# Kernel optimization log

Measured on AMD Instinct MI355X. Metric: run time of the kernel, lower is better.

## Reference

```python
import jax, jax.numpy as jnp
import numpy as np
import math

# Model dims (DeepSeek-V2 style, N reduced to 32 heads)
S = 2048       # tokens (single causal prefill sequence)
H = 5120       # hidden size
N = 32         # heads
P = 128        # qk nope head dim
R = 64         # qk rope head dim
V = 128        # v head dim
LQ = 1536      # q lora rank
LKV = 512      # kv lora rank
QK = P + R
EPS = 1e-6
BASE = 10000.0
FACTOR = 40.0
ORIG_MAX = 4096
BETA_FAST, BETA_SLOW = 32, 1

def _yarn_get_mscale(scale, mscale=1.0):
    if scale <= 1:
        return 1.0
    return 0.1 * mscale * math.log(scale) + 1.0

# softmax scale includes mscale^2 (mscale_all_dim=1.0)
SCALE = (QK ** -0.5) * _yarn_get_mscale(FACTOR, 1.0) ** 2
# cos/sin multiplier: yarn_get_mscale(f, mscale)/yarn_get_mscale(f, mscale_all_dim) = 1.0 here
MSCALE_COS = _yarn_get_mscale(FACTOR, 1.0) / _yarn_get_mscale(FACTOR, 1.0)

def _yarn_inv_freq():
    half = R // 2
    pos_freqs = BASE ** (np.arange(0, R, 2, dtype=np.float64) / R)
    extrapolation = 1.0 / pos_freqs
    interpolation = 1.0 / (FACTOR * pos_freqs)
    def corr_dim(n_rot):
        return R * math.log(ORIG_MAX / (n_rot * 2 * math.pi)) / (2 * math.log(BASE))
    low = max(math.floor(corr_dim(BETA_FAST)), 0)
    high = min(math.ceil(corr_dim(BETA_SLOW)), R - 1)
    ramp = np.clip((np.arange(half, dtype=np.float64) - low) / max(high - low, 0.001), 0, 1)
    mask = 1.0 - ramp  # extrapolation mask
    inv_freq = interpolation * (1 - mask) + extrapolation * mask
    return jnp.asarray(inv_freq, dtype=jnp.float32)

INV_FREQ = _yarn_inv_freq()  # (R//2,)

def _rms_norm(x, w):
    var = jnp.mean(x * x, axis=-1, keepdims=True)
    return x * jax.lax.rsqrt(var + EPS) * w

def _apply_rope_gptj(x, cos, sin):
    # non-neox (interleaved-pair) rotation; x: (..., R), cos/sin broadcastable (..., R//2)
    x1 = x[..., 0::2]
    x2 = x[..., 1::2]
    o1 = x1 * cos - x2 * sin
    o2 = x2 * cos + x1 * sin
    return jnp.stack([o1, o2], axis=-1).reshape(x.shape)

def setup_inputs() -> dict:
    key = jax.random.key(0)
    ks = jax.random.split(key, 6)
    s = 0.02
    return {
        "positions": jnp.arange(S, dtype=jnp.int64 if jax.config.jax_enable_x64 else jnp.int32),
        "hidden_states": jax.random.normal(ks[0], (S, H), dtype=jnp.float32),
        "w_qa": jax.random.normal(ks[1], (H, LQ), dtype=jnp.float32) * s,
        "q_a_ln_w": jnp.ones((LQ,), dtype=jnp.float32),
        "w_qb": jax.random.normal(ks[2], (LQ, N * QK), dtype=jnp.float32) * s,
        "w_kva": jax.random.normal(ks[3], (H, LKV + R), dtype=jnp.float32) * s,
        "kv_a_ln_w": jnp.ones((LKV,), dtype=jnp.float32),
        "w_kvb": jax.random.normal(ks[4], (LKV, N * (P + V)), dtype=jnp.float32) * s,
        "w_o": jax.random.normal(ks[5], (N * V, H), dtype=jnp.float32) * s,
    }

def reference(positions, hidden_states, w_qa, q_a_ln_w, w_qb, w_kva, kv_a_ln_w, w_kvb, w_o):
    # --- Q path: down-proj -> RMSNorm -> up-proj ---
    q_lat = _rms_norm(hidden_states @ w_qa, q_a_ln_w)             # (S, LQ)
    q = (q_lat @ w_qb).reshape(S, N, QK)                          # (S, N, P+R)
    q_nope, q_pe = q[..., :P], q[..., P:]
    # --- KV path: joint down-proj, split, norm kv_a, up-proj ---
    latent = hidden_states @ w_kva                                # (S, LKV+R)
    kv_a, k_pe = latent[:, :LKV], latent[:, LKV:]
    kv_a = _rms_norm(kv_a, kv_a_ln_w)
    kv = (kv_a @ w_kvb).reshape(S, N, P + V)
    k_nope, v = kv[..., :P], kv[..., P:]
    # --- partial RoPE (yarn, non-neox) on q_pe, k_pe ---
    freqs = positions.astype(jnp.float32)[:, None] * INV_FREQ     # (S, R//2)
    cos = jnp.cos(freqs) * MSCALE_COS
    sin = jnp.sin(freqs) * MSCALE_COS
    q_pe = _apply_rope_gptj(q_pe, cos[:, None, :], sin[:, None, :])  # (S, N, R)
    k_pe = _apply_rope_gptj(k_pe, cos, sin)                          # (S, R)
    # --- assemble q, k and run causal MHA ---
    q_full = jnp.concatenate([q_nope, q_pe], axis=-1)             # (S, N, QK)
    k_full = jnp.concatenate(
        [k_nope, jnp.broadcast_to(k_pe[:, None, :], (S, N, R))], axis=-1)
    scores = jnp.einsum('snd,tnd->nst', q_full, k_full) * SCALE   # (N, S, S)
    causal = jnp.tril(jnp.ones((S, S), dtype=bool))
    scores = jnp.where(causal[None], scores, jnp.finfo(scores.dtype).min)
    probs = jax.nn.softmax(scores, axis=-1)
    attn = jnp.einsum('nst,tnv->snv', probs, v)                   # (S, N, V)
    out = attn.reshape(S, N * V) @ w_o                            # (S, H)
    return out
```

## Files before the change

### kernel.cpp

```cpp
#include <hip/hip_runtime.h>
#include <hip/hip_bf16.h>
#include <math.h>

#define DEVI __device__ __forceinline__

typedef __bf16 bf16x8 __attribute__((ext_vector_type(8)));
typedef float f32x4 __attribute__((ext_vector_type(4)));

#define MFMA16(a, b, c) __builtin_amdgcn_mfma_f32_16x16x32_bf16((a), (b), (c), 0, 0, 0)

struct RopeConsts { float inv_freq[32]; };

DEVI float bfbits2f(unsigned int u) { union { unsigned int i; float f; } x; x.i = u << 16; return x.f; }
DEVI unsigned short f2bfbits(float f) {
    __hip_bfloat16 h = __float2bfloat16(f);
    unsigned short u; __builtin_memcpy(&u, &h, 2); return u;
}

DEVI void gl_lds16(const __hip_bfloat16* g, __hip_bfloat16* l) {
    __builtin_amdgcn_global_load_lds((const __attribute__((address_space(1))) void*)g,
                                     (__attribute__((address_space(3))) void*)l, 16, 0, 0);
}

__global__ void k_cvt_f32_bf16(const float* __restrict__ s, __hip_bfloat16* __restrict__ d, long n) {
    long i = ((long)blockIdx.x * 256 + threadIdx.x) * 4;
    if (i >= n) return;
    float4 f = *(const float4*)(s + i);
    ushort4 o = make_ushort4(f2bfbits(f.x), f2bfbits(f.y), f2bfbits(f.z), f2bfbits(f.w));
    *(ushort4*)((unsigned short*)d + i) = o;
}

struct TransBatch {
    const float* src[5];
    __hip_bfloat16* dst[5];
    int K[5], N[5], nbx[5];
    int boff[6];
};

__global__ __launch_bounds__(256)
void k_transpose_batch(TransBatch tbp) {
    __shared__ float tile[128][33];
    const int b = blockIdx.x;
    int seg = 0;
    if (b >= tbp.boff[1]) seg = 1;
    if (b >= tbp.boff[2]) seg = 2;
    if (b >= tbp.boff[3]) seg = 3;
    if (b >= tbp.boff[4]) seg = 4;
    const int local = b - tbp.boff[seg];
    const int nbx = tbp.nbx[seg];
    const int K = tbp.K[seg], N = tbp.N[seg];
    const float* __restrict__ src = tbp.src[seg];
    __hip_bfloat16* __restrict__ dst = tbp.dst[seg];
    const int nb = (local % nbx) * 32, kb = (local / nbx) * 128;

    const int tx = threadIdx.x & 31, ty = threadIdx.x >> 5;
    #pragma unroll
    for (int r = 0; r < 128; r += 8) {
        int k = kb + r + ty, n = nb + tx;
        tile[r + ty][tx] = (n < N) ? src[(size_t)k * N + n] : 0.0f;
    }
    __syncthreads();
    const int nl = threadIdx.x >> 3;
    const int kq = (threadIdx.x & 7) << 4;
    unsigned short* drow = (unsigned short*)(dst + (size_t)(nb + nl) * K + kb + kq);
    #pragma unroll
    for (int j4 = 0; j4 < 4; ++j4) {
        ushort4 o;
        o.x = f2bfbits(tile[kq + j4 * 4 + 0][nl]);
        o.y = f2bfbits(tile[kq + j4 * 4 + 1][nl]);
        o.z = f2bfbits(tile[kq + j4 * 4 + 2][nl]);
        o.w = f2bfbits(tile[kq + j4 * 4 + 3][nl]);
        *(ushort4*)(drow + j4 * 4) = o;
    }
}

DEVI void storeC(float* C, size_t i, float v) { C[i] = v; }
DEVI void storeC(__hip_bfloat16* C, size_t i, float v) { C[i] = __float2bfloat16(v); }

template <int NI, typename CT>
__global__ __launch_bounds__(512, 2)
void k_gemm128w(const __hip_bfloat16* __restrict__ A, int lda,
                const __hip_bfloat16* __restrict__ Bt,
                CT* __restrict__ C, int N, int K, float alpha) {
    extern __shared__ __hip_bfloat16 sm[];
    __hip_bfloat16* As = sm;
    __hip_bfloat16* Bs = sm + 16384;
    const int tid = threadIdx.x;
    const int lane = tid & 63, wave = tid >> 6;
    const int wm = wave >> 2, wn = wave & 3;
    const size_t bm = (size_t)blockIdx.y * 128, bn = (size_t)blockIdx.x * (64 * NI);

    const int srow8 = lane >> 3;
    const int sch = (lane & 7) ^ srow8;
    const __hip_bfloat16* Agb = A + (bm + wave * 8 + srow8) * (size_t)lda + (sch << 3);
    const __hip_bfloat16* Bgb = Bt + (bn + wave * 8 + srow8) * (size_t)K + (sch << 3);
    __hip_bfloat16* AsW = As + wave * 512;
    __hip_bfloat16* BsW = Bs + wave * 512;

    auto stage = [&](int buf, int kt) {
        #pragma unroll
        for (int i = 0; i < 2; ++i)
            gl_lds16(Agb + (size_t)i * 64 * lda + kt, AsW + buf * 8192 + i * 4096);
        #pragma unroll
        for (int i = 0; i < NI; ++i)
            gl_lds16(Bgb + (size_t)i * 64 * K + kt, BsW + buf * (NI * 4096) + i * 4096);
    };

    int aoff[4], boff[NI];
    #pragma unroll
    for (int mi = 0; mi < 4; ++mi) {
        int r = wm * 64 + mi * 16 + (lane & 15);
        aoff[mi] = r * 64 + (((lane >> 4) ^ (r & 7)) << 3);
    }
    #pragma unroll
    for (int ni = 0; ni < NI; ++ni) {
        int r = wn * (16 * NI) + ni * 16 + (lane & 15);
        boff[ni] = r * 64 + (((lane >> 4) ^ (r & 7)) << 3);
    }

    f32x4 acc[4][NI] = {};
    const int NT = K >> 6;

    stage(0, 0);
    stage(1, 64);
    asm volatile("s_waitcnt vmcnt(%0)" :: "n"(2 + NI) : "memory");
    __builtin_amdgcn_s_barrier();
    __builtin_amdgcn_sched_barrier(0);

    for (int t = 0; t < NT; ++t) {
        const int b = t & 1;
        const __hip_bfloat16* Ab = As + b * 8192;
        const __hip_bfloat16* Bb = Bs + b * (NI * 4096);
        bf16x8 af[4], bfr[NI];

        #pragma unroll
        for (int mi = 0; mi < 4; ++mi) af[mi] = *(const bf16x8*)(Ab + aoff[mi]);
        #pragma unroll
        for (int ni = 0; ni < NI; ++ni) bfr[ni] = *(const bf16x8*)(Bb + boff[ni]);
        __builtin_amdgcn_s_setprio(1);
        #pragma unroll
        for (int mi = 0; mi < 4; ++mi)
            #pragma unroll
            for (int ni = 0; ni < NI; ++ni)
                acc[mi][ni] = MFMA16(af[mi], bfr[ni], acc[mi][ni]);
        __builtin_amdgcn_s_setprio(0);

        #pragma unroll
        for (int mi = 0; mi < 4; ++mi) af[mi] = *(const bf16x8*)(Ab + (aoff[mi] ^ 32));
        #pragma unroll
        for (int ni = 0; ni < NI; ++ni) bfr[ni] = *(const bf16x8*)(Bb + (boff[ni] ^ 32));
        __builtin_amdgcn_s_setprio(1);
        #pragma unroll
        for (int mi = 0; mi < 4; ++mi)
            #pragma unroll
            for (int ni = 0; ni < NI; ++ni)
                acc[mi][ni] = MFMA16(af[mi], bfr[ni], acc[mi][ni]);
        __builtin_amdgcn_s_setprio(0);

        __builtin_amdgcn_sched_barrier(0);
        __builtin_amdgcn_s_barrier();
        if (t + 2 < NT) {
            stage(b, (t + 2) << 6);
            asm volatile("s_waitcnt vmcnt(%0)" :: "n"(2 + NI) : "memory");
        } else {
            asm volatile("s_waitcnt vmcnt(0)" ::: "memory");
        }
        __builtin_amdgcn_s_barrier();
        __builtin_amdgcn_sched_barrier(0);
    }

    const int row0 = (int)bm + wm * 64 + ((lane >> 4) << 2);
    const int col0 = (int)bn + wn * (16 * NI) + (lane & 15);
    #pragma unroll
    for (int mi = 0; mi < 4; ++mi)
        #pragma unroll
        for (int ni = 0; ni < NI; ++ni)
            #pragma unroll
            for (int r = 0; r < 4; ++r)
                storeC(C, (size_t)(row0 + mi * 16 + r) * N + (col0 + ni * 16), acc[mi][ni][r] * alpha);
}

template <typename CT>
__global__ __launch_bounds__(256, 2)
void k_gemm128p(const __hip_bfloat16* __restrict__ A, int lda,
                const __hip_bfloat16* __restrict__ Bt,
                CT* __restrict__ C, int N, int K, float alpha) {
    __shared__ __hip_bfloat16 As[2 * 8192];
    __shared__ __hip_bfloat16 Bs[2 * 8192];
    const int tid = threadIdx.x;
    const int lane = tid & 63, wave = tid >> 6;
    const int wm = wave >> 1, wn = wave & 1;
    const size_t bm = (size_t)blockIdx.y * 128, bn = (size_t)blockIdx.x * 128;

    const int srow8 = lane >> 3;
    const int sch = (lane & 7) ^ srow8;
    const __hip_bfloat16* Agb = A + (bm + wave * 8 + srow8) * (size_t)lda + (sch << 3);
    const __hip_bfloat16* Bgb = Bt + (bn + wave * 8 + srow8) * (size_t)K + (sch << 3);
    __hip_bfloat16* AsW = As + wave * 512;
    __hip_bfloat16* BsW = Bs + wave * 512;

    auto stage = [&](int buf, int kt) {
        #pragma unroll
        for (int i = 0; i < 4; ++i)
            gl_lds16(Agb + (size_t)i * 32 * lda + kt, AsW + buf * 8192 + i * 2048);
        #pragma unroll
        for (int i = 0; i < 4; ++i)
            gl_lds16(Bgb + (size_t)i * 32 * K + kt, BsW + buf * 8192 + i * 2048);
    };

    int aoff[4], boff[4];
    #pragma unroll
    for (int mi = 0; mi < 4; ++mi) {
        int r = wm * 64 + mi * 16 + (lane & 15);
        aoff[mi] = r * 64 + (((lane >> 4) ^ (r & 7)) << 3);
    }
    #pragma unroll
    for (int ni = 0; ni < 4; ++ni) {
        int r = wn * 64 + ni * 16 + (lane & 15);
        boff[ni] = r * 64 + (((lane >> 4) ^ (r & 7)) << 3);
    }

    f32x4 acc[4][4] = {};
    const int NT = K >> 6;

    stage(0, 0);
    stage(1, 64);
    asm volatile("s_waitcnt vmcnt(8)" ::: "memory");
    __builtin_amdgcn_s_barrier();
    __builtin_amdgcn_sched_barrier(0);

    for (int t = 0; t < NT; ++t) {
        const int b = t & 1;
        const __hip_bfloat16* Ab = As + b * 8192;
        const __hip_bfloat16* Bb = Bs + b * 8192;
        bf16x8 af[4], bfr[4];

        #pragma unroll
        for (int mi = 0; mi < 4; ++mi) af[mi] = *(const bf16x8*)(Ab + aoff[mi]);
        #pragma unroll
        for (int ni = 0; ni < 4; ++ni) bfr[ni] = *(const bf16x8*)(Bb + boff[ni]);
        __builtin_amdgcn_s_setprio(1);
        #pragma unroll
        for (int mi = 0; mi < 4; ++mi)
            #pragma unroll
            for (int ni = 0; ni < 4; ++ni)
                acc[mi][ni] = MFMA16(af[mi], bfr[ni], acc[mi][ni]);
        __builtin_amdgcn_s_setprio(0);

        #pragma unroll
        for (int mi = 0; mi < 4; ++mi) af[mi] = *(const bf16x8*)(Ab + (aoff[mi] ^ 32));
        #pragma unroll
        for (int ni = 0; ni < 4; ++ni) bfr[ni] = *(const bf16x8*)(Bb + (boff[ni] ^ 32));
        __builtin_amdgcn_s_setprio(1);
        #pragma unroll
        for (int mi = 0; mi < 4; ++mi)
            #pragma unroll
            for (int ni = 0; ni < 4; ++ni)
                acc[mi][ni] = MFMA16(af[mi], bfr[ni], acc[mi][ni]);
        __builtin_amdgcn_s_setprio(0);

        __builtin_amdgcn_sched_barrier(0);
        __builtin_amdgcn_s_barrier();
        if (t + 2 < NT) {
            stage(b, (t + 2) << 6);
            asm volatile("s_waitcnt vmcnt(8)" ::: "memory");
        } else {
            asm volatile("s_waitcnt vmcnt(0)" ::: "memory");
        }
        __builtin_amdgcn_s_barrier();
        __builtin_amdgcn_sched_barrier(0);
    }

    const int row0 = (int)bm + wm * 64 + ((lane >> 4) << 2);
    const int col0 = (int)bn + wn * 64 + (lane & 15);
    #pragma unroll
    for (int mi = 0; mi < 4; ++mi)
        #pragma unroll
        for (int ni = 0; ni < 4; ++ni)
            #pragma unroll
            for (int r = 0; r < 4; ++r)
                storeC(C, (size_t)(row0 + mi * 16 + r) * N + (col0 + ni * 16), acc[mi][ni][r] * alpha);
}

template <typename CT>
__global__ __launch_bounds__(512, 2)
void k_gemm256(const __hip_bfloat16* __restrict__ A, int lda,
               const __hip_bfloat16* __restrict__ Bt,
               CT* __restrict__ C, int N, int K) {
    extern __shared__ __hip_bfloat16 sm[];
    __hip_bfloat16* As = sm;
    __hip_bfloat16* Bs = sm + 32768;
    const int tid = threadIdx.x;
    const int lane = tid & 63, wave = tid >> 6;
    const int wm = wave >> 2, wn = wave & 3;
    const size_t bm = (size_t)blockIdx.y * 256, bn = (size_t)blockIdx.x * 256;

    const int srow8 = lane >> 3;
    const int sch = (lane & 7) ^ srow8;
    const __hip_bfloat16* Agb = A + (bm + wave * 8 + srow8) * (size_t)lda + (sch << 3);
    const __hip_bfloat16* Bgb = Bt + (bn + wave * 8 + srow8) * (size_t)K + (sch << 3);
    __hip_bfloat16* AsW = As + wave * 512;
    __hip_bfloat16* BsW = Bs + wave * 512;

    auto stage = [&](int buf, int kt) {
        #pragma unroll
        for (int i = 0; i < 4; ++i)
            gl_lds16(Agb + (size_t)i * 64 * lda + kt, AsW + buf * 16384 + i * 4096);
        #pragma unroll
        for (int i = 0; i < 4; ++i)
            gl_lds16(Bgb + (size_t)i * 64 * K + kt, BsW + buf * 16384 + i * 4096);
    };

    int aoff[8], boff[4];
    #pragma unroll
    for (int mi = 0; mi < 8; ++mi) {
        int r = wm * 128 + mi * 16 + (lane & 15);
        aoff[mi] = r * 64 + (((lane >> 4) ^ (r & 7)) << 3);
    }
    #pragma unroll
    for (int ni = 0; ni < 4; ++ni) {
        int r = wn * 64 + ni * 16 + (lane & 15);
        boff[ni] = r * 64 + (((lane >> 4) ^ (r & 7)) << 3);
    }

    f32x4 acc[8][4] = {};
    const int NT = K >> 6;

    stage(0, 0);
    stage(1, 64);
    asm volatile("s_waitcnt vmcnt(8)" ::: "memory");
    __builtin_amdgcn_s_barrier();
    __builtin_amdgcn_sched_barrier(0);

    for (int t = 0; t < NT; ++t) {
        const int b = t & 1;
        const __hip_bfloat16* Ab = As + b * 16384;
        const __hip_bfloat16* Bb = Bs + b * 16384;
        bf16x8 af[8], bfr[4];

        #pragma unroll
        for (int mi = 0; mi < 8; ++mi) af[mi] = *(const bf16x8*)(Ab + aoff[mi]);
        #pragma unroll
        for (int ni = 0; ni < 4; ++ni) bfr[ni] = *(const bf16x8*)(Bb + boff[ni]);
        __builtin_amdgcn_s_setprio(1);
        #pragma unroll
        for (int mi = 0; mi < 8; ++mi)
            #pragma unroll
            for (int ni = 0; ni < 4; ++ni)
                acc[mi][ni] = MFMA16(af[mi], bfr[ni], acc[mi][ni]);
        __builtin_amdgcn_s_setprio(0);

        #pragma unroll
        for (int mi = 0; mi < 8; ++mi) af[mi] = *(const bf16x8*)(Ab + (aoff[mi] ^ 32));
        #pragma unroll
        for (int ni = 0; ni < 4; ++ni) bfr[ni] = *(const bf16x8*)(Bb + (boff[ni] ^ 32));
        __builtin_amdgcn_s_setprio(1);
        #pragma unroll
        for (int mi = 0; mi < 8; ++mi)
            #pragma unroll
            for (int ni = 0; ni < 4; ++ni)
                acc[mi][ni] = MFMA16(af[mi], bfr[ni], acc[mi][ni]);
        __builtin_amdgcn_s_setprio(0);

        __builtin_amdgcn_sched_barrier(0);
        __builtin_amdgcn_s_barrier();
        if (t + 2 < NT) {
            stage(b, (t + 2) << 6);
            asm volatile("s_waitcnt vmcnt(8)" ::: "memory");
        } else {
            asm volatile("s_waitcnt vmcnt(0)" ::: "memory");
        }
        __builtin_amdgcn_s_barrier();
        __builtin_amdgcn_sched_barrier(0);
    }

    const int row0 = (int)bm + wm * 128 + ((lane >> 4) << 2);
    const int col0 = (int)bn + wn * 64 + (lane & 15);
    #pragma unroll
    for (int mi = 0; mi < 8; ++mi)
        #pragma unroll
        for (int ni = 0; ni < 4; ++ni)
            #pragma unroll
            for (int r = 0; r < 4; ++r)
                storeC(C, (size_t)(row0 + mi * 16 + r) * N + (col0 + ni * 16), acc[mi][ni][r]);
}

__global__ __launch_bounds__(256)
void k_rmsnorm2(__hip_bfloat16* base, int stride,
                const float* __restrict__ w0, int D0,
                int off1, const float* __restrict__ w1, int D1) {
    const int row = blockIdx.x;
    const int which = blockIdx.y;
    const float* w = which ? w1 : w0;
    const int D = which ? D1 : D0;
    unsigned int* xr = (unsigned int*)(base + (size_t)row * stride + (which ? off1 : 0));
    const int tid = threadIdx.x;
    const int n2 = D >> 1;
    float a[3], b[3];
    float ss = 0.0f;
    int c = 0;
    for (int i = tid; i < n2; i += 256) {
        unsigned int v = xr[i];
        float lo = bfbits2f(v & 0xffffu), hi = bfbits2f(v >> 16);
        a[c] = lo; b[c] = hi; ++c;
        ss += lo * lo + hi * hi;
    }
    #pragma unroll
    for (int d = 1; d < 64; d <<= 1) ss += __shfl_xor(ss, d, 64);
    __shared__ float red[4];
    if ((tid & 63) == 0) red[tid >> 6] = ss;
    __syncthreads();
    ss = red[0] + red[1] + red[2] + red[3];
    const float rs = rsqrtf(ss / (float)D + 1e-6f);
    c = 0;
    for (int i = tid; i < n2; i += 256) {
        float lo = a[c] * rs * w[2 * i], hi = b[c] * rs * w[2 * i + 1];
        xr[i] = (unsigned int)f2bfbits(lo) | ((unsigned int)f2bfbits(hi) << 16);
        ++c;
    }
}

__global__ __launch_bounds__(256)
void k_rope(__hip_bfloat16* __restrict__ q, __hip_bfloat16* __restrict__ latent, int lstride,
            const int* __restrict__ positions, RopeConsts rc) {
    __shared__ float2 scs[32];
    const int s = blockIdx.x, tid = threadIdx.x;
    if (tid < 32) {
        float fr = (float)positions[s] * rc.inv_freq[tid];
        float sn, cn;
        sincosf(fr, &sn, &cn);
        scs[tid] = make_float2(cn, sn);
    }
    __syncthreads();
    #pragma unroll
    for (int p = tid; p < 1024; p += 256) {
        int head = p >> 5, i = p & 31;
        float2 c = scs[i];
        unsigned int* b = (unsigned int*)(q + (size_t)s * 6144 + head * 192 + 128 + 2 * i);
        unsigned int v = *b;
        float x1 = bfbits2f(v & 0xffffu), x2 = bfbits2f(v >> 16);
        float o1 = x1 * c.x - x2 * c.y, o2 = x2 * c.x + x1 * c.y;
        *b = (unsigned int)f2bfbits(o1) | ((unsigned int)f2bfbits(o2) << 16);
    }
    if (tid < 32) {
        float2 c = scs[tid];
        unsigned int* b = (unsigned int*)(latent + (size_t)s * lstride + 512 + 2 * tid);
        unsigned int v = *b;
        float x1 = bfbits2f(v & 0xffffu), x2 = bfbits2f(v >> 16);
        float o1 = x1 * c.x - x2 * c.y, o2 = x2 * c.x + x1 * c.y;
        *b = (unsigned int)f2bfbits(o1) | ((unsigned int)f2bfbits(o2) << 16);
    }
}

__global__ __launch_bounds__(256)
void k_vtrans(const __hip_bfloat16* __restrict__ kv, __hip_bfloat16* __restrict__ vt) {
    __shared__ unsigned int tile[128][33];
    const int h = blockIdx.z, t0 = blockIdx.x * 128, v0 = blockIdx.y * 32;
    const int tx = threadIdx.x & 31, ty = threadIdx.x >> 5;
    const unsigned short* kvu = (const unsigned short*)kv;
    #pragma unroll
    for (int r = 0; r < 128; r += 8) {
        int t = t0 + r + ty;
        tile[r + ty][tx] = kvu[(size_t)t * 8192 + h * 256 + 128 + v0 + tx];
    }
    __syncthreads();
    const int vl = threadIdx.x >> 3;
    const int tq = (threadIdx.x & 7) << 4;
    unsigned short* drow = (unsigned short*)(vt + ((size_t)h * 128 + v0 + vl) * 2048 + t0 + tq);
    #pragma unroll
    for (int j4 = 0; j4 < 4; ++j4) {
        ushort4 o;
        o.x = (unsigned short)tile[tq + j4 * 4 + 0][vl];
        o.y = (unsigned short)tile[tq + j4 * 4 + 1][vl];
        o.z = (unsigned short)tile[tq + j4 * 4 + 2][vl];
        o.w = (unsigned short)tile[tq + j4 * 4 + 3][vl];
        *(ushort4*)(drow + j4 * 4) = o;
    }
}

template <int NBUF>
__global__ __launch_bounds__(512, 1)
void k_attn(const __hip_bfloat16* __restrict__ q,
            const __hip_bfloat16* __restrict__ kv,
            const __hip_bfloat16* __restrict__ latent,
            int lstride,
            const __hip_bfloat16* __restrict__ vt,
            __hip_bfloat16* __restrict__ attnout) {
    extern __shared__ __hip_bfloat16 smem[];
    __hip_bfloat16* KN = smem;
    __hip_bfloat16* KP = KN + NBUF * 8192;
    __hip_bfloat16* VT = KP + NBUF * 4096;
    __hip_bfloat16* P  = VT + NBUF * 8192;

    const int h = blockIdx.x & 31;
    const int pr = (int)(blockIdx.x >> 5);
    const int tid = threadIdx.x;
    const int lane = tid & 63, wave = tid >> 6;
    const int l15 = lane & 15, rquad = lane >> 4;
    const int qrw0 = pr * 128 + wave * 16;
    const int qrw1 = (15 - pr) * 128 + wave * 16;
    const int nt0 = 2 * pr + 2;
    const int nt  = 2 * (15 - pr) + 2;

    auto stage = [&](int buf, int t0) {
        #pragma unroll
        for (int p = 0; p < 2; ++p) {
            int s = p * 512 + tid;
            int row = s >> 4, ch = s & 15;
            gl_lds16(kv + (size_t)(t0 + row) * 8192 + h * 256 + ((ch ^ (row & 7)) << 3),
                     KN + buf * 8192 + p * 4096 + wave * 512);
        }
        {
            int row = tid >> 3, ch = tid & 7;
            gl_lds16(latent + (size_t)(t0 + row) * lstride + 512 + ((ch ^ (row & 7)) << 3),
                     KP + buf * 4096 + wave * 512);
        }
        #pragma unroll
        for (int p = 0; p < 2; ++p) {
            int s = p * 512 + tid;
            int row = s >> 3, ch = s & 7;
            gl_lds16(vt + ((size_t)h * 128 + row) * 2048 + t0 + ((ch ^ (row & 7)) << 3),
                     VT + buf * 8192 + p * 4096 + wave * 512);
        }
    };

    bf16x8 qf[2][6];
    {
        const __hip_bfloat16* qrow0 = q + (size_t)(qrw0 + l15) * 6144 + h * 192 + (rquad << 3);
        const __hip_bfloat16* qrow1 = q + (size_t)(qrw1 + l15) * 6144 + h * 192 + (rquad << 3);
        #pragma unroll
        for (int f = 0; f < 6; ++f) {
            qf[0][f] = *(const bf16x8*)(qrow0 + f * 32);
            qf[1][f] = *(const bf16x8*)(qrow1 + f * 32);
        }
    }

    f32x4 o[2][8] = {};
    float mi_[2][4], li[2][4];
    #pragma unroll
    for (int rb = 0; rb < 2; ++rb)
        #pragma unroll
        for (int r = 0; r < 4; ++r) { mi_[rb][r] = -1e30f; li[rb][r] = 0.0f; }

    int cur = 0;

    stage(0, 0);
    stage(1, 64);
    asm volatile("s_waitcnt vmcnt(5)" ::: "memory");
    __builtin_amdgcn_s_barrier();
    __builtin_amdgcn_sched_barrier(0);

    for (int tt = 0; tt < nt; ++tt) {
        const int t0 = tt * 64;
        const bool act0 = tt < nt0;
        if (NBUF == 3) cur = tt % 3;

        if (NBUF == 3 && tt + 2 < nt) stage((tt + 2) % 3, t0 + 128);

        f32x4 s[2][4] = {};
        #pragma unroll
        for (int tb = 0; tb < 4; ++tb) {
            const int rbk = tb * 16 + l15;
            const __hip_bfloat16* knb = KN + cur * 8192 + rbk * 128;
            const __hip_bfloat16* kpb = KP + cur * 4096 + rbk * 64;
            bf16x8 kf[6];
            #pragma unroll
            for (int f = 0; f < 4; ++f)
                kf[f] = *(const bf16x8*)(knb + (((rquad + f * 4) ^ (rbk & 7)) << 3));
            #pragma unroll
            for (int f = 0; f < 2; ++f)
                kf[4 + f] = *(const bf16x8*)(kpb + (((rquad + f * 4) ^ (rbk & 7)) << 3));
            #pragma unroll
            for (int f = 0; f < 6; ++f)
                s[1][tb] = MFMA16(qf[1][f], kf[f], s[1][tb]);
            if (act0)
                #pragma unroll
                for (int f = 0; f < 6; ++f)
                    s[0][tb] = MFMA16(qf[0][f], kf[f], s[0][tb]);
        }

        #pragma unroll
        for (int rb = 0; rb < 2; ++rb) {
            if (rb == 0 && !act0) continue;
            const int qr = rb ? qrw1 : qrw0;
            if (t0 + 63 > qr) {
                const int tcol = t0 + l15;
                const int qrow0_ = qr + (rquad << 2);
                #pragma unroll
                for (int tb = 0; tb < 4; ++tb)
                    #pragma unroll
                    for (int r = 0; r < 4; ++r)
                        if (tcol + tb * 16 > qrow0_ + r) s[rb][tb][r] = -1e30f;
            }
            float pm[4];
            #pragma unroll
            for (int r = 0; r < 4; ++r) {
                float v = fmaxf(fmaxf(s[rb][0][r], s[rb][1][r]), fmaxf(s[rb][2][r], s[rb][3][r]));
                v = fmaxf(v, __shfl_xor(v, 1)); v = fmaxf(v, __shfl_xor(v, 2));
                v = fmaxf(v, __shfl_xor(v, 4)); v = fmaxf(v, __shfl_xor(v, 8));
                pm[r] = v;
            }
            bool need = (pm[0] > mi_[rb][0] + 24.0f) || (pm[1] > mi_[rb][1] + 24.0f) ||
                        (pm[2] > mi_[rb][2] + 24.0f) || (pm[3] > mi_[rb][3] + 24.0f);
            if (__any(need ? 1 : 0)) {
                float sf[4];
                #pragma unroll
                for (int r = 0; r < 4; ++r) {
                    float mn = fmaxf(mi_[rb][r], pm[r]);
                    sf[r] = exp2f(mi_[rb][r] - mn);
                    mi_[rb][r] = mn;
                    li[rb][r] *= sf[r];
                }
                #pragma unroll
                for (int vb = 0; vb < 8; ++vb)
                    #pragma unroll
                    for (int r = 0; r < 4; ++r) o[rb][vb][r] *= sf[r];
            }

            #pragma unroll
            for (int tb = 0; tb < 4; ++tb)
                #pragma unroll
                for (int r = 0; r < 4; ++r) {
                    float p = exp2f(s[rb][tb][r] - mi_[rb][r]);
                    li[rb][r] += p;
                    P[wave * 2304 + (rb * 16 + (rquad << 2) + r) * 72 + tb * 16 + l15] = __float2bfloat16(p);
                }
        }

        #pragma unroll
        for (int kk = 0; kk < 2; ++kk) {
            bf16x8 pf0 = *(const bf16x8*)&P[wave * 2304 + l15 * 72 + kk * 32 + (rquad << 3)];
            bf16x8 pf1 = *(const bf16x8*)&P[wave * 2304 + (16 + l15) * 72 + kk * 32 + (rquad << 3)];
            #pragma unroll
            for (int vb = 0; vb < 8; ++vb) {
                const int vrow = vb * 16 + l15;
                bf16x8 vf = *(const bf16x8*)(VT + cur * 8192 + vrow * 64 + (((rquad + kk * 4) ^ (vrow & 7)) << 3));
                o[1][vb] = MFMA16(pf1, vf, o[1][vb]);
                if (act0) o[0][vb] = MFMA16(pf0, vf, o[0][vb]);
            }
        }

        if (NBUF == 3) {
            __builtin_amdgcn_sched_barrier(0);
            if (tt + 2 < nt) asm volatile("s_waitcnt vmcnt(5)" ::: "memory");
            else             asm volatile("s_waitcnt vmcnt(0)" ::: "memory");
            __builtin_amdgcn_s_barrier();
            __builtin_amdgcn_sched_barrier(0);
        } else {
            __builtin_amdgcn_sched_barrier(0);
            __builtin_amdgcn_s_barrier();
            if (tt + 2 < nt) {
                stage(cur, t0 + 128);
                asm volatile("s_waitcnt vmcnt(5)" ::: "memory");
            } else {
                asm volatile("s_waitcnt vmcnt(0)" ::: "memory");
            }
            __builtin_amdgcn_s_barrier();
            __builtin_amdgcn_sched_barrier(0);
            cur ^= 1;
        }
    }

    #pragma unroll
    for (int rb = 0; rb < 2; ++rb)
        #pragma unroll
        for (int r = 0; r < 4; ++r) {
            float v = li[rb][r];
            v += __shfl_xor(v, 1); v += __shfl_xor(v, 2);
            v += __shfl_xor(v, 4); v += __shfl_xor(v, 8);
            const float inv = 1.0f / v;
            const int row = (rb ? qrw1 : qrw0) + (rquad << 2) + r;
            __hip_bfloat16* orow = attnout + (size_t)row * 4096 + h * 128 + l15;
            #pragma unroll
            for (int vb = 0; vb < 8; ++vb) orow[vb * 16] = __float2bfloat16(o[rb][vb][r] * inv);
        }
}

extern "C" void kernel_launch(void* const* d_in, const int* in_sizes, int n_in,
                              void* d_out, int out_size, void* d_ws, size_t ws_size,
                              hipStream_t stream) {
    const int* positions   = (const int*)d_in[0];
    const float* hidden    = (const float*)d_in[1];
    const float* w_qa      = (const float*)d_in[2];
    const float* q_a_ln_w  = (const float*)d_in[3];
    const float* w_qb      = (const float*)d_in[4];
    const float* w_kva     = (const float*)d_in[5];
    const float* kv_a_ln_w = (const float*)d_in[6];
    const float* w_kvb     = (const float*)d_in[7];
    const float* w_o       = (const float*)d_in[8];
    float* out = (float*)d_out;

    char* ws = (char*)d_ws;
    size_t off = 0;
    auto alloc = [&](size_t n) { char* p = ws + off; off += (n + 255) & ~(size_t)255; return p; };
    __hip_bfloat16* h_bf    = (__hip_bfloat16*)alloc(2048ull * 5120 * 2);
    __hip_bfloat16* wqakva  = (__hip_bfloat16*)alloc(2176ull * 5120 * 2);
    __hip_bfloat16* wqb_t   = (__hip_bfloat16*)alloc(6144ull * 1536 * 2);
    __hip_bfloat16* wkvb_t  = (__hip_bfloat16*)alloc(8192ull * 512 * 2);
    __hip_bfloat16* wo_t    = (__hip_bfloat16*)alloc(5120ull * 4096 * 2);
    __hip_bfloat16* qlatc   = (__hip_bfloat16*)alloc(2048ull * 2176 * 2);
    __hip_bfloat16* qbuf    = (__hip_bfloat16*)alloc(2048ull * 6144 * 2);
    __hip_bfloat16* kvb     = (__hip_bfloat16*)alloc(2048ull * 8192 * 2);
    __hip_bfloat16* vtb     = (__hip_bfloat16*)alloc(32ull * 128 * 2048 * 2);
    __hip_bfloat16* attnb   = (__hip_bfloat16*)alloc(2048ull * 4096 * 2);
    __hip_bfloat16* q_lat   = qlatc;
    __hip_bfloat16* latent  = qlatc + 1536;
    const int LSTR = 2176;
    (void)ws_size; (void)in_sizes; (void)n_in; (void)out_size;

    double mscale = 0.1 * log(40.0) + 1.0;
    float scale = (float)(pow(192.0, -0.5) * mscale * mscale);
    float scale2 = scale * 1.44269504088896f;
    RopeConsts rc;
    {
        const double PI = 3.14159265358979323846;
        double lowd = floor(64.0 * log(4096.0 / (32.0 * 2.0 * PI)) / (2.0 * log(10000.0)));
        double highd = ceil(64.0 * log(4096.0 / (1.0 * 2.0 * PI)) / (2.0 * log(10000.0)));
        if (lowd < 0.0) lowd = 0.0;
        if (highd > 63.0) highd = 63.0;
        double denom = (highd - lowd) > 0.001 ? (highd - lowd) : 0.001;
        for (int i = 0; i < 32; ++i) {
            double pf = pow(10000.0, (2.0 * i) / 64.0);
            double extra = 1.0 / pf, inter = 1.0 / (40.0 * pf);
            double ramp = ((double)i - lowd) / denom;
            ramp = ramp < 0.0 ? 0.0 : (ramp > 1.0 ? 1.0 : ramp);
            double mask = 1.0 - ramp;
            rc.inv_freq[i] = (float)(inter * (1.0 - mask) + extra * mask);
        }
    }

    bool ok256 =
        (hipFuncSetAttribute(reinterpret_cast<const void*>(k_gemm256<__hip_bfloat16>),
                             hipFuncAttributeMaxDynamicSharedMemorySize, 131072) == hipSuccess);
    bool okW2 =
        (hipFuncSetAttribute(reinterpret_cast<const void*>(k_gemm128w<2, __hip_bfloat16>),
                             hipFuncAttributeMaxDynamicSharedMemorySize, 65536) == hipSuccess);
    bool okW5 =
        (hipFuncSetAttribute(reinterpret_cast<const void*>(k_gemm128w<5, float>),
                             hipFuncAttributeMaxDynamicSharedMemorySize, 114688) == hipSuccess);
    bool okW6 =
        (hipFuncSetAttribute(reinterpret_cast<const void*>(k_gemm128w<6, __hip_bfloat16>),
                             hipFuncAttributeMaxDynamicSharedMemorySize, 131072) == hipSuccess);

    k_cvt_f32_bf16<<<(2048 * 5120) / 1024, 256, 0, stream>>>(hidden, h_bf, 2048L * 5120);
    {
        TransBatch tb;
        tb.src[0] = w_qa;  tb.dst[0] = wqakva;                    tb.K[0] = 5120; tb.N[0] = 1536; tb.nbx[0] = 48;
        tb.src[1] = w_kva; tb.dst[1] = wqakva + 1536ull * 5120;   tb.K[1] = 5120; tb.N[1] = 576;  tb.nbx[1] = 20;
        tb.src[2] = w_qb;  tb.dst[2] = wqb_t;                     tb.K[2] = 1536; tb.N[2] = 6144; tb.nbx[2] = 192;
        tb.src[3] = w_kvb; tb.dst[3] = wkvb_t;                    tb.K[3] = 512;  tb.N[3] = 8192; tb.nbx[3] = 256;
        tb.src[4] = w_o;   tb.dst[4] = wo_t;                      tb.K[4] = 4096; tb.N[4] = 5120; tb.nbx[4] = 160;
        int nb0 = 48 * 40, nb1 = 20 * 40, nb2 = 192 * 12, nb3 = 256 * 4, nb4 = 160 * 32;
        tb.boff[0] = 0;
        tb.boff[1] = nb0;
        tb.boff[2] = nb0 + nb1;
        tb.boff[3] = nb0 + nb1 + nb2;
        tb.boff[4] = nb0 + nb1 + nb2 + nb3;
        tb.boff[5] = nb0 + nb1 + nb2 + nb3 + nb4;
        k_transpose_batch<<<tb.boff[5], 256, 0, stream>>>(tb);
    }

    if (okW2)
        k_gemm128w<2, __hip_bfloat16><<<dim3(17, 16), 512, 65536, stream>>>(h_bf, 5120, wqakva, qlatc, 2176, 5120, 1.0f);
    else
        k_gemm128p<__hip_bfloat16><<<dim3(17, 16), 256, 0, stream>>>(h_bf, 5120, wqakva, qlatc, 2176, 5120, 1.0f);
    k_rmsnorm2<<<dim3(2048, 2), 256, 0, stream>>>(qlatc, LSTR, q_a_ln_w, 1536, 1536, kv_a_ln_w, 512);

    if (okW6)
        k_gemm128w<6, __hip_bfloat16><<<dim3(16, 16), 512, 131072, stream>>>(q_lat, LSTR, wqb_t, qbuf, 6144, 1536, scale2);
    else
        k_gemm128p<__hip_bfloat16><<<dim3(48, 16), 256, 0, stream>>>(q_lat, LSTR, wqb_t, qbuf, 6144, 1536, scale2);

    k_rope<<<2048, 256, 0, stream>>>(qbuf, latent, LSTR, positions, rc);
    if (ok256)
        k_gemm256<__hip_bfloat16><<<dim3(32, 8), 512, 131072, stream>>>(latent, LSTR, wkvb_t, kvb, 8192, 512);
    else
        k_gemm128p<__hip_bfloat16><<<dim3(64, 16), 256, 0, stream>>>(latent, LSTR, wkvb_t, kvb, 8192, 512, 1.0f);
    k_vtrans<<<dim3(16, 4, 32), 256, 0, stream>>>(kvb, vtb);

    {
        hipError_t fe = hipFuncSetAttribute(reinterpret_cast<const void*>(k_attn<3>),
                                            hipFuncAttributeMaxDynamicSharedMemorySize, 159744);
        if (fe == hipSuccess) {
            k_attn<3><<<256, 512, 159744, stream>>>(qbuf, kvb, latent, LSTR, vtb, attnb);
        } else {
            hipFuncSetAttribute(reinterpret_cast<const void*>(k_attn<2>),
                                hipFuncAttributeMaxDynamicSharedMemorySize, 118784);
            k_attn<2><<<256, 512, 118784, stream>>>(qbuf, kvb, latent, LSTR, vtb, attnb);
        }
    }

    if (okW5)
        k_gemm128w<5, float><<<dim3(16, 16), 512, 114688, stream>>>(attnb, 4096, wo_t, out, 5120, 4096, 1.0f);
    else
        k_gemm128p<float><<<dim3(40, 16), 256, 0, stream>>>(attnb, 4096, wo_t, out, 5120, 4096, 1.0f);
}
```

Measured before the change: 416.9 us.

## Replace paired-block triple-buffered attention with one-qblock-per-CTA single-buffer kernel

The attention kernel no longer pairs a short and a long causal query block in one CTA with a three-stage async LDS pipeline. Each CTA now handles one 128-row query block with a single LDS buffer, twice as many CTAs (512), and launch bounds that allow two CTAs per CU. Parallelism and occupancy rise, and latency hiding comes from co-resident CTAs instead of explicit prefetch. In exchange, loads are no longer overlapped within a CTA, K/V tiles are loaded twice as often overall, and workload balance across CTAs is uneven, with heavy blocks scheduled first.

```diff
diff --git a/kernel.cpp b/kernel.cpp
--- a/kernel.cpp
+++ b/kernel.cpp
@@ -478,202 +478,146 @@
     }
 }
 
-template <int NBUF>
-__global__ __launch_bounds__(512, 1)
-void k_attn(const __hip_bfloat16* __restrict__ q,
-            const __hip_bfloat16* __restrict__ kv,
-            const __hip_bfloat16* __restrict__ latent,
-            int lstride,
-            const __hip_bfloat16* __restrict__ vt,
-            __hip_bfloat16* __restrict__ attnout) {
-    extern __shared__ __hip_bfloat16 smem[];
-    __hip_bfloat16* KN = smem;
-    __hip_bfloat16* KP = KN + NBUF * 8192;
-    __hip_bfloat16* VT = KP + NBUF * 4096;
-    __hip_bfloat16* P  = VT + NBUF * 8192;
+__global__ __launch_bounds__(512, 2)
+void k_attn2(const __hip_bfloat16* __restrict__ q,
+             const __hip_bfloat16* __restrict__ kv,
+             const __hip_bfloat16* __restrict__ latent,
+             int lstride,
+             const __hip_bfloat16* __restrict__ vt,
+             __hip_bfloat16* __restrict__ attnout) {
+    __shared__ __hip_bfloat16 KN[8192];
+    __shared__ __hip_bfloat16 KP[4096];
+    __shared__ __hip_bfloat16 VT[8192];
+    __shared__ __hip_bfloat16 P[9216];
 
     const int h = blockIdx.x & 31;
-    const int pr = (int)(blockIdx.x >> 5);
+    const int qb = 15 - (int)(blockIdx.x >> 5);
     const int tid = threadIdx.x;
     const int lane = tid & 63, wave = tid >> 6;
     const int l15 = lane & 15, rquad = lane >> 4;
-    const int qrw0 = pr * 128 + wave * 16;
-    const int qrw1 = (15 - pr) * 128 + wave * 16;
-    const int nt0 = 2 * pr + 2;
-    const int nt  = 2 * (15 - pr) + 2;
-
-    auto stage = [&](int buf, int t0) {
+    const int qrw = qb * 128 + wave * 16;
+    const int nt = 2 * qb + 2;
+
+    auto stage = [&](int t0) {
         #pragma unroll
         for (int p = 0; p < 2; ++p) {
             int s = p * 512 + tid;
             int row = s >> 4, ch = s & 15;
             gl_lds16(kv + (size_t)(t0 + row) * 8192 + h * 256 + ((ch ^ (row & 7)) << 3),
-                     KN + buf * 8192 + p * 4096 + wave * 512);
+                     KN + p * 4096 + wave * 512);
         }
         {
             int row = tid >> 3, ch = tid & 7;
             gl_lds16(latent + (size_t)(t0 + row) * lstride + 512 + ((ch ^ (row & 7)) << 3),
-                     KP + buf * 4096 + wave * 512);
+                     KP + wave * 512);
         }
         #pragma unroll
         for (int p = 0; p < 2; ++p) {
             int s = p * 512 + tid;
             int row = s >> 3, ch = s & 7;
             gl_lds16(vt + ((size_t)h * 128 + row) * 2048 + t0 + ((ch ^ (row & 7)) << 3),
-                     VT + buf * 8192 + p * 4096 + wave * 512);
+                     VT + p * 4096 + wave * 512);
         }
     };
 
-    bf16x8 qf[2][6];
+    bf16x8 qf[6];
     {
-        const __hip_bfloat16* qrow0 = q + (size_t)(qrw0 + l15) * 6144 + h * 192 + (rquad << 3);
-        const __hip_bfloat16* qrow1 = q + (size_t)(qrw1 + l15) * 6144 + h * 192 + (rquad << 3);
-        #pragma unroll
-        for (int f = 0; f < 6; ++f) {
-            qf[0][f] = *(const bf16x8*)(qrow0 + f * 32);
-            qf[1][f] = *(const bf16x8*)(qrow1 + f * 32);
-        }
-    }
-
-    f32x4 o[2][8] = {};
-    float mi_[2][4], li[2][4];
-    #pragma unroll
-    for (int rb = 0; rb < 2; ++rb)
-        #pragma unroll
-        for (int r = 0; r < 4; ++r) { mi_[rb][r] = -1e30f; li[rb][r] = 0.0f; }
-
-    int cur = 0;
-
-    stage(0, 0);
-    stage(1, 64);
-    asm volatile("s_waitcnt vmcnt(5)" ::: "memory");
-    __builtin_amdgcn_s_barrier();
-    __builtin_amdgcn_sched_barrier(0);
+        const __hip_bfloat16* qrow = q + (size_t)(qrw + l15) * 6144 + h * 192 + (rquad << 3);
+        #pragma unroll
+        for (int f = 0; f < 6; ++f) qf[f] = *(const bf16x8*)(qrow + f * 32);
+    }
+
+    f32x4 o[8] = {};
+    float mi_[4], li[4];
+    #pragma unroll
+    for (int r = 0; r < 4; ++r) { mi_[r] = -1e30f; li[r] = 0.0f; }
 
     for (int tt = 0; tt < nt; ++tt) {
         const int t0 = tt * 64;
-        const bool act0 = tt < nt0;
-        if (NBUF == 3) cur = tt % 3;
-
-        if (NBUF == 3 && tt + 2 < nt) stage((tt + 2) % 3, t0 + 128);
-
-        f32x4 s[2][4] = {};
+        stage(t0);
+        __syncthreads();
+
+        f32x4 s[4] = {};
         #pragma unroll
         for (int tb = 0; tb < 4; ++tb) {
             const int rbk = tb * 16 + l15;
-            const __hip_bfloat16* knb = KN + cur * 8192 + rbk * 128;
-            const __hip_bfloat16* kpb = KP + cur * 4096 + rbk * 64;
-            bf16x8 kf[6];
+            const __hip_bfloat16* knb = KN + rbk * 128;
+            const __hip_bfloat16* kpb = KP + rbk * 64;
             #pragma unroll
             for (int f = 0; f < 4; ++f)
-                kf[f] = *(const bf16x8*)(knb + (((rquad + f * 4) ^ (rbk & 7)) << 3));
+                s[tb] = MFMA16(qf[f], *(const bf16x8*)(knb + (((rquad + f * 4) ^ (rbk & 7)) << 3)), s[tb]);
             #pragma unroll
             for (int f = 0; f < 2; ++f)
-                kf[4 + f] = *(const bf16x8*)(kpb + (((rquad + f * 4) ^ (rbk & 7)) << 3));
-            #pragma unroll
-            for (int f = 0; f < 6; ++f)
-                s[1][tb] = MFMA16(qf[1][f], kf[f], s[1][tb]);
-            if (act0)
-                #pragma unroll
-                for (int f = 0; f < 6; ++f)
-                    s[0][tb] = MFMA16(qf[0][f], kf[f], s[0][tb]);
-        }
-
-        #pragma unroll
-        for (int rb = 0; rb < 2; ++rb) {
-            if (rb == 0 && !act0) continue;
-            const int qr = rb ? qrw1 : qrw0;
-            if (t0 + 63 > qr) {
-                const int tcol = t0 + l15;
-                const int qrow0_ = qr + (rquad << 2);
-                #pragma unroll
-                for (int tb = 0; tb < 4; ++tb)
-                    #pragma unroll
-                    for (int r = 0; r < 4; ++r)
-                        if (tcol + tb * 16 > qrow0_ + r) s[rb][tb][r] = -1e30f;
-            }
-            float pm[4];
-            #pragma unroll
-            for (int r = 0; r < 4; ++r) {
-                float v = fmaxf(fmaxf(s[rb][0][r], s[rb][1][r]), fmaxf(s[rb][2][r], s[rb][3][r]));
-                v = fmaxf(v, __shfl_xor(v, 1)); v = fmaxf(v, __shfl_xor(v, 2));
-                v = fmaxf(v, __shfl_xor(v, 4)); v = fmaxf(v, __shfl_xor(v, 8));
-                pm[r] = v;
-            }
-            bool need = (pm[0] > mi_[rb][0] + 24.0f) || (pm[1] > mi_[rb][1] + 24.0f) ||
-                        (pm[2] > mi_[rb][2] + 24.0f) || (pm[3] > mi_[rb][3] + 24.0f);
-            if (__any(need ? 1 : 0)) {
-                float sf[4];
-                #pragma unroll
-                for (int r = 0; r < 4; ++r) {
-                    float mn = fmaxf(mi_[rb][r], pm[r]);
-                    sf[r] = exp2f(mi_[rb][r] - mn);
-                    mi_[rb][r] = mn;
-                    li[rb][r] *= sf[r];
-                }
-                #pragma unroll
-                for (int vb = 0; vb < 8; ++vb)
-                    #pragma unroll
-                    for (int r = 0; r < 4; ++r) o[rb][vb][r] *= sf[r];
-            }
-
+                s[tb] = MFMA16(qf[4 + f], *(const bf16x8*)(kpb + (((rquad + f * 4) ^ (rbk & 7)) << 3)), s[tb]);
+        }
+
+        if (t0 + 63 > qrw) {
+            const int tcol = t0 + l15;
+            const int qrow0_ = qrw + (rquad << 2);
             #pragma unroll
             for (int tb = 0; tb < 4; ++tb)
                 #pragma unroll
-                for (int r = 0; r < 4; ++r) {
-                    float p = exp2f(s[rb][tb][r] - mi_[rb][r]);
-                    li[rb][r] += p;
-                    P[wave * 2304 + (rb * 16 + (rquad << 2) + r) * 72 + tb * 16 + l15] = __float2bfloat16(p);
-                }
-        }
+                for (int r = 0; r < 4; ++r)
+                    if (tcol + tb * 16 > qrow0_ + r) s[tb][r] = -1e30f;
+        }
+        float pm[4];
+        #pragma unroll
+        for (int r = 0; r < 4; ++r) {
+            float v = fmaxf(fmaxf(s[0][r], s[1][r]), fmaxf(s[2][r], s[3][r]));
+            v = fmaxf(v, __shfl_xor(v, 1)); v = fmaxf(v, __shfl_xor(v, 2));
+            v = fmaxf(v, __shfl_xor(v, 4)); v = fmaxf(v, __shfl_xor(v, 8));
+            pm[r] = v;
+        }
+        bool need = (pm[0] > mi_[0] + 24.0f) || (pm[1] > mi_[1] + 24.0f) ||
+                    (pm[2] > mi_[2] + 24.0f) || (pm[3] > mi_[3] + 24.0f);
+        if (__any(need ? 1 : 0)) {
+            float sf[4];
+            #pragma unroll
+            for (int r = 0; r < 4; ++r) {
+                float mn = fmaxf(mi_[r], pm[r]);
+                sf[r] = exp2f(mi_[r] - mn);
+                mi_[r] = mn;
+                li[r] *= sf[r];
+            }
+            #pragma unroll
+            for (int vb = 0; vb < 8; ++vb)
+                #pragma unroll
+                for (int r = 0; r < 4; ++r) o[vb][r] *= sf[r];
+        }
+        #pragma unroll
+        for (int tb = 0; tb < 4; ++tb)
+            #pragma unroll
+            for (int r = 0; r < 4; ++r) {
+                float p = exp2f(s[tb][r] - mi_[r]);
+                li[r] += p;
+                P[wave * 1152 + ((rquad << 2) + r) * 72 + tb * 16 + l15] = __float2bfloat16(p);
+            }
 
         #pragma unroll
         for (int kk = 0; kk < 2; ++kk) {
-            bf16x8 pf0 = *(const bf16x8*)&P[wave * 2304 + l15 * 72 + kk * 32 + (rquad << 3)];
-            bf16x8 pf1 = *(const bf16x8*)&P[wave * 2304 + (16 + l15) * 72 + kk * 32 + (rquad << 3)];
+            bf16x8 pf = *(const bf16x8*)&P[wave * 1152 + l15 * 72 + kk * 32 + (rquad << 3)];
             #pragma unroll
             for (int vb = 0; vb < 8; ++vb) {
                 const int vrow = vb * 16 + l15;
-                bf16x8 vf = *(const bf16x8*)(VT + cur * 8192 + vrow * 64 + (((rquad + kk * 4) ^ (vrow & 7)) << 3));
-                o[1][vb] = MFMA16(pf1, vf, o[1][vb]);
-                if (act0) o[0][vb] = MFMA16(pf0, vf, o[0][vb]);
+                bf16x8 vf = *(const bf16x8*)(VT + vrow * 64 + (((rquad + kk * 4) ^ (vrow & 7)) << 3));
+                o[vb] = MFMA16(pf, vf, o[vb]);
             }
         }
 
-        if (NBUF == 3) {
-            __builtin_amdgcn_sched_barrier(0);
-            if (tt + 2 < nt) asm volatile("s_waitcnt vmcnt(5)" ::: "memory");
-            else             asm volatile("s_waitcnt vmcnt(0)" ::: "memory");
-            __builtin_amdgcn_s_barrier();
-            __builtin_amdgcn_sched_barrier(0);
-        } else {
-            __builtin_amdgcn_sched_barrier(0);
-            __builtin_amdgcn_s_barrier();
-            if (tt + 2 < nt) {
-                stage(cur, t0 + 128);
-                asm volatile("s_waitcnt vmcnt(5)" ::: "memory");
-            } else {
-                asm volatile("s_waitcnt vmcnt(0)" ::: "memory");
-            }
-            __builtin_amdgcn_s_barrier();
-            __builtin_amdgcn_sched_barrier(0);
-            cur ^= 1;
-        }
-    }
-
-    #pragma unroll
-    for (int rb = 0; rb < 2; ++rb)
-        #pragma unroll
-        for (int r = 0; r < 4; ++r) {
-            float v = li[rb][r];
-            v += __shfl_xor(v, 1); v += __shfl_xor(v, 2);
-            v += __shfl_xor(v, 4); v += __shfl_xor(v, 8);
-            const float inv = 1.0f / v;
-            const int row = (rb ? qrw1 : qrw0) + (rquad << 2) + r;
-            __hip_bfloat16* orow = attnout + (size_t)row * 4096 + h * 128 + l15;
-            #pragma unroll
-            for (int vb = 0; vb < 8; ++vb) orow[vb * 16] = __float2bfloat16(o[rb][vb][r] * inv);
-        }
+        __syncthreads();
+    }
+
+    #pragma unroll
+    for (int r = 0; r < 4; ++r) {
+        float v = li[r];
+        v += __shfl_xor(v, 1); v += __shfl_xor(v, 2);
+        v += __shfl_xor(v, 4); v += __shfl_xor(v, 8);
+        const float inv = 1.0f / v;
+        const int row = qrw + (rquad << 2) + r;
+        __hip_bfloat16* orow = attnout + (size_t)row * 4096 + h * 128 + l15;
+        #pragma unroll
+        for (int vb = 0; vb < 8; ++vb) orow[vb * 16] = __float2bfloat16(o[vb][r] * inv);
+    }
 }
 
 extern "C" void kernel_launch(void* const* d_in, const int* in_sizes, int n_in,
@@ -778,17 +722,7 @@
         k_gemm128p<__hip_bfloat16><<<dim3(64, 16), 256, 0, stream>>>(latent, LSTR, wkvb_t, kvb, 8192, 512, 1.0f);
     k_vtrans<<<dim3(16, 4, 32), 256, 0, stream>>>(kvb, vtb);
 
-    {
-        hipError_t fe = hipFuncSetAttribute(reinterpret_cast<const void*>(k_attn<3>),
-                                            hipFuncAttributeMaxDynamicSharedMemorySize, 159744);
-        if (fe == hipSuccess) {
-            k_attn<3><<<256, 512, 159744, stream>>>(qbuf, kvb, latent, LSTR, vtb, attnb);
-        } else {
-            hipFuncSetAttribute(reinterpret_cast<const void*>(k_attn<2>),
-                                hipFuncAttributeMaxDynamicSharedMemorySize, 118784);
-            k_attn<2><<<256, 512, 118784, stream>>>(qbuf, kvb, latent, LSTR, vtb, attnb);
-        }
-    }
+    k_attn2<<<512, 512, 0, stream>>>(qbuf, kvb, latent, LSTR, vtb, attnb);
 
     if (okW5)
         k_gemm128w<5, float><<<dim3(16, 16), 512, 114688, stream>>>(attnb, 4096, wo_t, out, 5120, 4096, 1.0f);
```

After: 424.1 us. Within noise of the previous version (+1.7%).
